# Kernel optimization log

Measured on AMD Instinct MI355X. Metric: run time of the kernel, lower is better.

The kernel has to match this reference:

```python
import jax, jax.numpy as jnp
import numpy as np

HIDDEN = 128
OUT_EMB = 256
OUT_CH = 1
NUM_LAYERS = 3
NUM_EDGES = 1000000
NUM_NODES = 50000


def glorot_orthogonal(key, shape, scale=2.0):
    # orthogonal init then rescale variance like DIG's glorot_orthogonal
    W = jax.nn.initializers.orthogonal()(key, shape, jnp.float32)
    W = W * jnp.sqrt(scale / ((shape[0] + shape[1]) * jnp.var(W)))
    return W


def setup_inputs() -> dict:
    key = jax.random.key(0)
    ks = jax.random.split(key, 8)
    e2 = jax.random.normal(ks[0], (NUM_EDGES, HIDDEN), dtype=jnp.float32)
    i = jax.random.randint(ks[1], (NUM_EDGES,), 0, NUM_NODES, dtype=jnp.int64)
    W_up = glorot_orthogonal(ks[2], (OUT_EMB, HIDDEN))
    b_up = jnp.zeros((OUT_EMB,), jnp.float32)
    Ws = jnp.stack([glorot_orthogonal(k, (OUT_EMB, OUT_EMB)) for k in jax.random.split(ks[3], NUM_LAYERS)])
    bs = jnp.zeros((NUM_LAYERS, OUT_EMB), jnp.float32)
    W_out = glorot_orthogonal(ks[4], (OUT_CH, OUT_EMB))
    return {"e2": e2, "i": i, "W_up": W_up, "b_up": b_up,
            "Ws": Ws, "bs": bs, "W_out": W_out, "num_nodes": NUM_NODES}


def reference(e2, i, W_up, b_up, Ws, bs, W_out, num_nodes):
    # scatter-sum edge messages into nodes: v[n] = sum_{k: i[k]==n} e2[k]
    v = jax.ops.segment_sum(e2, i, num_segments=num_nodes)  # [N, HIDDEN]
    v = v @ W_up.T + b_up                                   # [N, OUT_EMB]
    for l in range(NUM_LAYERS):
        v = jax.nn.silu(v @ Ws[l].T + bs[l])
    return v @ W_out.T                                      # [N, OUT_CH]
```

## Files before the change

kernel.cpp:

```cpp
#include <hip/hip_runtime.h>

#define HIDDEN 128
#define OUT_EMB 256
#define NLAYERS 3
#define TM 64
#define LDA 264

typedef __bf16 bf16x8 __attribute__((ext_vector_type(8)));
typedef float f32x4 __attribute__((ext_vector_type(4)));

__device__ __forceinline__ unsigned short f2bf(float x) {
    union { float f; unsigned u; } c; c.f = x;
    unsigned r = c.u + 0x7fff + ((c.u >> 16) & 1);
    return (unsigned short)(r >> 16);
}
__device__ __forceinline__ float bf2f(unsigned short h) {
    union { unsigned u; float f; } c; c.u = ((unsigned)h) << 16;
    return c.f;
}
__device__ __forceinline__ unsigned pack2(float a, float b) {
    return (unsigned)f2bf(a) | ((unsigned)f2bf(b) << 16);
}

__global__ __launch_bounds__(256) void hist_convert_kernel(
    const int* __restrict__ idx, int* __restrict__ counts, int ne, int nbh,
    const float* __restrict__ wup_f, const float* __restrict__ ws_f,
    unsigned short* __restrict__ wup, unsigned short* __restrict__ wsl)
{
    if ((int)blockIdx.x < nbh) {
        int e = blockIdx.x * 256 + threadIdx.x;
        if (e < ne) atomicAdd(&counts[idx[e]], 1);
    } else {
        const int n1 = OUT_EMB * HIDDEN;
        const int n2 = NLAYERS * OUT_EMB * OUT_EMB;
        int t = (blockIdx.x - nbh) * 256 + threadIdx.x;
        int base = t * 4;
        if (base < n1) {
            f32x4 x = *(const f32x4*)(wup_f + base);
            uint2 p; p.x = pack2(x[0], x[1]); p.y = pack2(x[2], x[3]);
            *(uint2*)(wup + base) = p;
        } else if (base < n1 + n2) {
            int j = base - n1;
            f32x4 x = *(const f32x4*)(ws_f + j);
            uint2 p; p.x = pack2(x[0], x[1]); p.y = pack2(x[2], x[3]);
            *(uint2*)(wsl + j) = p;
        }
    }
}

__global__ __launch_bounds__(256) void scan1_kernel(
    const int* __restrict__ counts, int* __restrict__ bsum, int n)
{
    __shared__ int sh[256];
    int t = threadIdx.x;
    int i = blockIdx.x * 256 + t;
    sh[t] = (i < n) ? counts[i] : 0;
    __syncthreads();
    for (int off = 128; off > 0; off >>= 1) {
        if (t < off) sh[t] += sh[t + off];
        __syncthreads();
    }
    if (t == 0) bsum[blockIdx.x] = sh[0];
}

__global__ __launch_bounds__(256) void scan2_kernel(
    int* __restrict__ bsum, int* __restrict__ boff, int nb)
{
    __shared__ int sh[256];
    int t = threadIdx.x;
    int v = (t < nb) ? bsum[t] : 0;
    sh[t] = v;
    __syncthreads();
    for (int off = 1; off < 256; off <<= 1) {
        int u = (t >= off) ? sh[t - off] : 0;
        __syncthreads();
        sh[t] += u;
        __syncthreads();
    }
    if (t < nb) boff[t] = sh[t] - v;
}

__global__ __launch_bounds__(256) void scan3_kernel(
    const int* __restrict__ counts, const int* __restrict__ boff,
    int* __restrict__ offsets, int* __restrict__ cursor, int n)
{
    __shared__ int sh[256];
    int t = threadIdx.x;
    int i = blockIdx.x * 256 + t;
    int v = (i < n) ? counts[i] : 0;
    sh[t] = v;
    __syncthreads();
    for (int off = 1; off < 256; off <<= 1) {
        int u = (t >= off) ? sh[t - off] : 0;
        __syncthreads();
        sh[t] += u;
        __syncthreads();
    }
    if (i < n) {
        int excl = boff[blockIdx.x] + sh[t] - v;
        offsets[i] = excl;
        cursor[i]  = excl;
    }
}

__global__ __launch_bounds__(256) void fill_kernel(
    const int* __restrict__ idx, int* __restrict__ cursor,
    int* __restrict__ edge_list, int ne)
{
    int e = blockIdx.x * 256 + threadIdx.x;
    if (e < ne) {
        int pos = atomicAdd(&cursor[idx[e]], 1);
        edge_list[pos] = e;
    }
}

__global__ __launch_bounds__(256) void gather_kernel(
    const float* __restrict__ e2, const int* __restrict__ edge_list,
    const int* __restrict__ offsets, const int* __restrict__ counts,
    unsigned short* __restrict__ vbf, int Mpad)
{
    int node = blockIdx.x * 4 + (threadIdx.x >> 6);
    if (node >= Mpad) return;
    int lane = threadIdx.x & 63;
    int half = lane >> 5;
    int c4   = lane & 31;
    int start = offsets[node];
    int cnt   = counts[node];

    f32x4 a0 = {0.f, 0.f, 0.f, 0.f};
    f32x4 a1 = {0.f, 0.f, 0.f, 0.f};

    int j = 0;
    for (; j + 4 <= cnt; j += 4) {
        int e0 = edge_list[start + j + half];
        int e1 = edge_list[start + j + 2 + half];
        f32x4 x0 = __builtin_nontemporal_load((const f32x4*)(e2 + (long long)e0 * HIDDEN + c4 * 4));
        f32x4 x1 = __builtin_nontemporal_load((const f32x4*)(e2 + (long long)e1 * HIDDEN + c4 * 4));
        a0 += x0;
        a1 += x1;
    }
    for (; j + 2 <= cnt; j += 2) {
        int e0 = edge_list[start + j + half];
        f32x4 x0 = __builtin_nontemporal_load((const f32x4*)(e2 + (long long)e0 * HIDDEN + c4 * 4));
        a0 += x0;
    }
    if (j < cnt && half == 0) {
        int e0 = edge_list[start + j];
        f32x4 x0 = __builtin_nontemporal_load((const f32x4*)(e2 + (long long)e0 * HIDDEN + c4 * 4));
        a1 += x0;
    }
    a0 += a1;
    a0[0] += __shfl_xor(a0[0], 32);
    a0[1] += __shfl_xor(a0[1], 32);
    a0[2] += __shfl_xor(a0[2], 32);
    a0[3] += __shfl_xor(a0[3], 32);

    if (half == 0) {
        uint2 p; p.x = pack2(a0[0], a0[1]); p.y = pack2(a0[2], a0[3]);
        *(uint2*)(vbf + (long long)node * HIDDEN + c4 * 4) = p;
    }
}

__global__ __launch_bounds__(256) void mlp_kernel(
    const unsigned short* __restrict__ vbf,
    const unsigned short* __restrict__ wup,
    const float* __restrict__ bup,
    const unsigned short* __restrict__ wsl,
    const float* __restrict__ bs,
    const float* __restrict__ wout,
    float* __restrict__ out, int M)
{
    __shared__ unsigned short act[TM * LDA];

    const int tid  = threadIdx.x;
    const int wv   = tid >> 6;
    const int lane = tid & 63;
    const int ln15 = lane & 15;
    const int kq   = lane >> 4;
    const int n0   = wv * 64;
    const long long rowbase = (long long)blockIdx.x * TM;

    f32x4 acc[4][4];

    #pragma unroll
    for (int mt = 0; mt < 4; ++mt)
        #pragma unroll
        for (int nt = 0; nt < 4; ++nt)
            acc[mt][nt] = (f32x4){0.f, 0.f, 0.f, 0.f};

    #pragma unroll
    for (int ks = 0; ks < 4; ++ks) {
        bf16x8 a[4], w[4];
        #pragma unroll
        for (int mt = 0; mt < 4; ++mt)
            a[mt] = *(const bf16x8*)&vbf[(rowbase + mt * 16 + ln15) * HIDDEN + ks * 32 + kq * 8];
        #pragma unroll
        for (int nt = 0; nt < 4; ++nt)
            w[nt] = *(const bf16x8*)&wup[(n0 + nt * 16 + ln15) * HIDDEN + ks * 32 + kq * 8];
        #pragma unroll
        for (int mt = 0; mt < 4; ++mt)
            #pragma unroll
            for (int nt = 0; nt < 4; ++nt)
                acc[mt][nt] = __builtin_amdgcn_mfma_f32_16x16x32_bf16(w[nt], a[mt], acc[mt][nt], 0, 0, 0);
    }
    #pragma unroll
    for (int nt = 0; nt < 4; ++nt) {
        int nb4 = n0 + nt * 16 + kq * 4;
        f32x4 bi = *(const f32x4*)(bup + nb4);
        #pragma unroll
        for (int mt = 0; mt < 4; ++mt) {
            int row = mt * 16 + ln15;
            float x0 = acc[mt][nt][0] + bi[0];
            float x1 = acc[mt][nt][1] + bi[1];
            float x2 = acc[mt][nt][2] + bi[2];
            float x3 = acc[mt][nt][3] + bi[3];
            uint2 p; p.x = pack2(x0, x1); p.y = pack2(x2, x3);
            *(uint2*)&act[row * LDA + nb4] = p;
        }
    }
    __syncthreads();

    for (int l = 0; l < NLAYERS; ++l) {
        const unsigned short* W = wsl + l * OUT_EMB * OUT_EMB;
        const float* bias_l = bs + l * OUT_EMB;

        #pragma unroll
        for (int mt = 0; mt < 4; ++mt)
            #pragma unroll
            for (int nt = 0; nt < 4; ++nt)
                acc[mt][nt] = (f32x4){0.f, 0.f, 0.f, 0.f};

        #pragma unroll
        for (int ks = 0; ks < 8; ++ks) {
            bf16x8 a[4], w[4];
            #pragma unroll
            for (int mt = 0; mt < 4; ++mt)
                a[mt] = *(const bf16x8*)&act[(mt * 16 + ln15) * LDA + ks * 32 + kq * 8];
            #pragma unroll
            for (int nt = 0; nt < 4; ++nt)
                w[nt] = *(const bf16x8*)&W[(n0 + nt * 16 + ln15) * OUT_EMB + ks * 32 + kq * 8];
            #pragma unroll
            for (int mt = 0; mt < 4; ++mt)
                #pragma unroll
                for (int nt = 0; nt < 4; ++nt)
                    acc[mt][nt] = __builtin_amdgcn_mfma_f32_16x16x32_bf16(w[nt], a[mt], acc[mt][nt], 0, 0, 0);
        }
        __syncthreads();
        #pragma unroll
        for (int nt = 0; nt < 4; ++nt) {
            int nb4 = n0 + nt * 16 + kq * 4;
            f32x4 bi = *(const f32x4*)(bias_l + nb4);
            #pragma unroll
            for (int mt = 0; mt < 4; ++mt) {
                int row = mt * 16 + ln15;
                float x0 = acc[mt][nt][0] + bi[0];
                float x1 = acc[mt][nt][1] + bi[1];
                float x2 = acc[mt][nt][2] + bi[2];
                float x3 = acc[mt][nt][3] + bi[3];
                x0 = x0 / (1.f + __expf(-x0));
                x1 = x1 / (1.f + __expf(-x1));
                x2 = x2 / (1.f + __expf(-x2));
                x3 = x3 / (1.f + __expf(-x3));
                uint2 p; p.x = pack2(x0, x1); p.y = pack2(x2, x3);
                *(uint2*)&act[row * LDA + nb4] = p;
            }
        }
        __syncthreads();
    }

    {
        int r = tid >> 2;
        int part = tid & 3;
        const unsigned short* arow = &act[r * LDA + part * 64];
        const float* wrow = wout + part * 64;
        float s = 0.f;
        #pragma unroll
        for (int jj = 0; jj < 64; ++jj) s += bf2f(arow[jj]) * wrow[jj];
        s += __shfl_xor(s, 1);
        s += __shfl_xor(s, 2);
        long long rowg = rowbase + r;
        if (part == 0 && rowg < M) out[rowg] = s;
    }
}

extern "C" void kernel_launch(void* const* d_in, const int* in_sizes, int n_in,
                              void* d_out, int out_size, void* d_ws, size_t ws_size,
                              hipStream_t stream) {
    const float* e2    = (const float*)d_in[0];
    const int*   idx   = (const int*)d_in[1];
    const float* W_up  = (const float*)d_in[2];
    const float* b_up  = (const float*)d_in[3];
    const float* Ws    = (const float*)d_in[4];
    const float* bs    = (const float*)d_in[5];
    const float* W_out = (const float*)d_in[6];

    const int ne = in_sizes[0] / HIDDEN;
    const int M  = out_size;
    const int Mpad = ((M + TM - 1) / TM) * TM;
    const int nb = (Mpad + 255) / 256;

    char* p = (char*)d_ws;
    unsigned short* vbf    = (unsigned short*)p;  p += (size_t)Mpad * HIDDEN * 2;
    unsigned short* wup_bf = (unsigned short*)p;  p += (size_t)OUT_EMB * HIDDEN * 2;
    unsigned short* wsl_bf = (unsigned short*)p;  p += (size_t)NLAYERS * OUT_EMB * OUT_EMB * 2;
    int* counts    = (int*)p;  p += (size_t)Mpad * 4;
    int* offsets   = (int*)p;  p += (size_t)Mpad * 4;
    int* cursor    = (int*)p;  p += (size_t)Mpad * 4;
    int* bsum      = (int*)p;  p += 256 * 4;
    int* boff      = (int*)p;  p += 256 * 4;
    int* edge_list = (int*)p;  p += (size_t)ne * 4;

    hipMemsetAsync(counts, 0, (size_t)Mpad * 4, stream);

    {
        const int nbh = (ne + 255) / 256;
        const int total4 = (OUT_EMB * HIDDEN + NLAYERS * OUT_EMB * OUT_EMB) / 4;
        const int nbc = (total4 + 255) / 256;
        hist_convert_kernel<<<nbh + nbc, 256, 0, stream>>>(
            idx, counts, ne, nbh, W_up, Ws, wup_bf, wsl_bf);
    }
    scan1_kernel<<<nb, 256, 0, stream>>>(counts, bsum, Mpad);
    scan2_kernel<<<1, 256, 0, stream>>>(bsum, boff, nb);
    scan3_kernel<<<nb, 256, 0, stream>>>(counts, boff, offsets, cursor, Mpad);
    fill_kernel <<<(ne + 255) / 256, 256, 0, stream>>>(idx, cursor, edge_list, ne);

    gather_kernel<<<(Mpad + 3) / 4, 256, 0, stream>>>(e2, edge_list, offsets, counts, vbf, Mpad);

    mlp_kernel<<<Mpad / TM, 256, 0, stream>>>(vbf, wup_bf, b_up, wsl_bf, bs, W_out,
                                              (float*)d_out, M);
}
```

Before: 860.5 us.

## Fuse scan passes, deepen gather unroll, use fast reciprocal SiLU, vectorize output dot

Merges the single-block scan of block sums into the third scan kernel, so each block redundantly scans the block sums and one launch is removed. The gather loop now processes 8 edges per iteration, with four independent accumulators per half-wave, to keep more memory loads in flight. SiLU replaces its division with a hardware reciprocal, and the final output projection reads bf16x8 and float4 vectors instead of scalars. The redundant per-block scan adds a little work to every block, and the approximate reciprocal slightly changes numerics.

```diff
diff --git a/kernel.cpp b/kernel.cpp
--- a/kernel.cpp
+++ b/kernel.cpp
@@ -63,41 +63,28 @@
     if (t == 0) bsum[blockIdx.x] = sh[0];
 }
 
-__global__ __launch_bounds__(256) void scan2_kernel(
-    int* __restrict__ bsum, int* __restrict__ boff, int nb)
+__global__ __launch_bounds__(256) void scan3_kernel(
+    const int* __restrict__ counts, const int* __restrict__ bsum,
+    int* __restrict__ offsets, int* __restrict__ cursor, int n, int nb)
 {
     __shared__ int sh[256];
+    __shared__ int shb[256];
     int t = threadIdx.x;
-    int v = (t < nb) ? bsum[t] : 0;
-    sh[t] = v;
+    int i = blockIdx.x * 256 + t;
+    int v  = (i < n)  ? counts[i] : 0;
+    int bv = (t < nb) ? bsum[t]   : 0;
+    sh[t] = v; shb[t] = bv;
     __syncthreads();
     for (int off = 1; off < 256; off <<= 1) {
-        int u = (t >= off) ? sh[t - off] : 0;
-        __syncthreads();
-        sh[t] += u;
-        __syncthreads();
-    }
-    if (t < nb) boff[t] = sh[t] - v;
-}
-
-__global__ __launch_bounds__(256) void scan3_kernel(
-    const int* __restrict__ counts, const int* __restrict__ boff,
-    int* __restrict__ offsets, int* __restrict__ cursor, int n)
-{
-    __shared__ int sh[256];
-    int t = threadIdx.x;
-    int i = blockIdx.x * 256 + t;
-    int v = (i < n) ? counts[i] : 0;
-    sh[t] = v;
-    __syncthreads();
-    for (int off = 1; off < 256; off <<= 1) {
-        int u = (t >= off) ? sh[t - off] : 0;
-        __syncthreads();
-        sh[t] += u;
+        int u  = (t >= off) ? sh[t - off]  : 0;
+        int ub = (t >= off) ? shb[t - off] : 0;
+        __syncthreads();
+        sh[t] += u; shb[t] += ub;
         __syncthreads();
     }
     if (i < n) {
-        int excl = boff[blockIdx.x] + sh[t] - v;
+        int blockoff = (blockIdx.x > 0) ? shb[blockIdx.x - 1] : 0;
+        int excl = blockoff + sh[t] - v;
         offsets[i] = excl;
         cursor[i]  = excl;
     }
@@ -126,29 +113,41 @@
     int c4   = lane & 31;
     int start = offsets[node];
     int cnt   = counts[node];
+    const float* base = e2 + c4 * 4;
 
     f32x4 a0 = {0.f, 0.f, 0.f, 0.f};
     f32x4 a1 = {0.f, 0.f, 0.f, 0.f};
+    f32x4 a2 = {0.f, 0.f, 0.f, 0.f};
+    f32x4 a3 = {0.f, 0.f, 0.f, 0.f};
 
     int j = 0;
-    for (; j + 4 <= cnt; j += 4) {
-        int e0 = edge_list[start + j + half];
-        int e1 = edge_list[start + j + 2 + half];
-        f32x4 x0 = __builtin_nontemporal_load((const f32x4*)(e2 + (long long)e0 * HIDDEN + c4 * 4));
-        f32x4 x1 = __builtin_nontemporal_load((const f32x4*)(e2 + (long long)e1 * HIDDEN + c4 * 4));
+    for (; j + 8 <= cnt; j += 8) {
+        int b = start + j + half * 4;
+        int e0 = edge_list[b + 0];
+        int e1 = edge_list[b + 1];
+        int e2i = edge_list[b + 2];
+        int e3 = edge_list[b + 3];
+        f32x4 x0 = __builtin_nontemporal_load((const f32x4*)(base + (long long)e0  * HIDDEN));
+        f32x4 x1 = __builtin_nontemporal_load((const f32x4*)(base + (long long)e1  * HIDDEN));
+        f32x4 x2 = __builtin_nontemporal_load((const f32x4*)(base + (long long)e2i * HIDDEN));
+        f32x4 x3 = __builtin_nontemporal_load((const f32x4*)(base + (long long)e3  * HIDDEN));
         a0 += x0;
         a1 += x1;
+        a2 += x2;
+        a3 += x3;
     }
     for (; j + 2 <= cnt; j += 2) {
         int e0 = edge_list[start + j + half];
-        f32x4 x0 = __builtin_nontemporal_load((const f32x4*)(e2 + (long long)e0 * HIDDEN + c4 * 4));
+        f32x4 x0 = __builtin_nontemporal_load((const f32x4*)(base + (long long)e0 * HIDDEN));
         a0 += x0;
     }
     if (j < cnt && half == 0) {
         int e0 = edge_list[start + j];
-        f32x4 x0 = __builtin_nontemporal_load((const f32x4*)(e2 + (long long)e0 * HIDDEN + c4 * 4));
+        f32x4 x0 = __builtin_nontemporal_load((const f32x4*)(base + (long long)e0 * HIDDEN));
         a1 += x0;
     }
+    a0 += a2;
+    a1 += a3;
     a0 += a1;
     a0[0] += __shfl_xor(a0[0], 32);
     a0[1] += __shfl_xor(a0[1], 32);
@@ -257,10 +256,10 @@
                 float x1 = acc[mt][nt][1] + bi[1];
                 float x2 = acc[mt][nt][2] + bi[2];
                 float x3 = acc[mt][nt][3] + bi[3];
-                x0 = x0 / (1.f + __expf(-x0));
-                x1 = x1 / (1.f + __expf(-x1));
-                x2 = x2 / (1.f + __expf(-x2));
-                x3 = x3 / (1.f + __expf(-x3));
+                x0 = x0 * __builtin_amdgcn_rcpf(1.f + __expf(-x0));
+                x1 = x1 * __builtin_amdgcn_rcpf(1.f + __expf(-x1));
+                x2 = x2 * __builtin_amdgcn_rcpf(1.f + __expf(-x2));
+                x3 = x3 * __builtin_amdgcn_rcpf(1.f + __expf(-x3));
                 uint2 p; p.x = pack2(x0, x1); p.y = pack2(x2, x3);
                 *(uint2*)&act[row * LDA + nb4] = p;
             }
@@ -275,7 +274,15 @@
         const float* wrow = wout + part * 64;
         float s = 0.f;
         #pragma unroll
-        for (int jj = 0; jj < 64; ++jj) s += bf2f(arow[jj]) * wrow[jj];
+        for (int jj = 0; jj < 8; ++jj) {
+            bf16x8 v = *(const bf16x8*)&arow[jj * 8];
+            f32x4 w0 = *(const f32x4*)&wrow[jj * 8];
+            f32x4 w1 = *(const f32x4*)&wrow[jj * 8 + 4];
+            s += (float)v[0] * w0[0] + (float)v[1] * w0[1]
+               + (float)v[2] * w0[2] + (float)v[3] * w0[3]
+               + (float)v[4] * w1[0] + (float)v[5] * w1[1]
+               + (float)v[6] * w1[2] + (float)v[7] * w1[3];
+        }
         s += __shfl_xor(s, 1);
         s += __shfl_xor(s, 2);
         long long rowg = rowbase + r;
@@ -307,7 +314,6 @@
     int* offsets   = (int*)p;  p += (size_t)Mpad * 4;
     int* cursor    = (int*)p;  p += (size_t)Mpad * 4;
     int* bsum      = (int*)p;  p += 256 * 4;
-    int* boff      = (int*)p;  p += 256 * 4;
     int* edge_list = (int*)p;  p += (size_t)ne * 4;
 
     hipMemsetAsync(counts, 0, (size_t)Mpad * 4, stream);
@@ -320,8 +326,7 @@
             idx, counts, ne, nbh, W_up, Ws, wup_bf, wsl_bf);
     }
     scan1_kernel<<<nb, 256, 0, stream>>>(counts, bsum, Mpad);
-    scan2_kernel<<<1, 256, 0, stream>>>(bsum, boff, nb);
-    scan3_kernel<<<nb, 256, 0, stream>>>(counts, boff, offsets, cursor, Mpad);
+    scan3_kernel<<<nb, 256, 0, stream>>>(counts, bsum, offsets, cursor, Mpad, nb);
     fill_kernel <<<(ne + 255) / 256, 256, 0, stream>>>(idx, cursor, edge_list, ne);
 
     gather_kernel<<<(Mpad + 3) / 4, 256, 0, stream>>>(e2, edge_list, offsets, counts, vbf, Mpad);
```

After: 849.8 us. About the same (-1.2%).
